# Optimization experiments

Measured on AMD Instinct MI355X. Metric: run time of the kernel, lower is better.

The kernel has to match this reference:

```python
import jax, jax.numpy as jnp
import numpy as np

EPS = 1e-05


def setup_inputs() -> dict:
    key = jax.random.key(0)
    k0, k1, k2, k3, k4 = jax.random.split(key, 5)
    B, N, D = 8, 4096, 1024
    scale = 1.0 / np.sqrt(D)  # roughly xavier scale for D x D
    return {
        "x": jax.random.normal(k0, (B, N, D), dtype=jnp.float32),
        "w_query_real": jax.random.normal(k1, (D, D), dtype=jnp.float32) * scale,
        "w_query_imag": jax.random.normal(k2, (D, D), dtype=jnp.float32) * scale,
        "w_key": jax.random.normal(k3, (D, D), dtype=jnp.float32) * scale,
        "w_value": jax.random.normal(k4, (D, D), dtype=jnp.float32) * scale,
    }


def reference(x, w_query_real, w_query_imag, w_key, w_value):
    # x is real -> x_real = x_imag = x (torch fallback branch)
    q_real = jnp.einsum('bnd,de->bne', x, w_query_real)
    q_imag = jnp.einsum('bnd,de->bne', x, w_query_imag)
    query = jax.nn.relu(q_real) * jax.nn.relu(q_imag)  # relu gating; dropout p=0

    key = jnp.einsum('bnd,de->bne', x, w_key)
    value = jnp.einsum('bnd,de->bne', x, w_value)
    # L2 norm over the sequence axis (dim=1), keepdim
    key = key / (jnp.linalg.norm(key, axis=1, keepdims=True) + EPS)
    value = value / (jnp.linalg.norm(value, axis=1, keepdims=True) + EPS)

    kv_attn = jax.nn.relu(jnp.einsum('bnd,bne->bde', key, value))  # [B, D, D]
    return jnp.einsum('bnd,bde->bne', query, kv_attn)
```

## Files before the change

kernel.cpp:

```cpp
#include <hip/hip_runtime.h>
#include <stdint.h>
#include <stddef.h>

#define D_ 1024
#define NSEQ_ 4096
#define BATCH_ 8
#define BN_ (BATCH_ * NSEQ_)

typedef __attribute__((ext_vector_type(8))) short short8;
typedef __attribute__((ext_vector_type(4))) short short4_t;
typedef __attribute__((ext_vector_type(4))) float float4_t;

__device__ __forceinline__ short f2b(float f) {
  union { float f; uint32_t u; } x; x.f = f;
  uint32_t r = x.u + 0x7fffu + ((x.u >> 16) & 1u);
  return (short)(r >> 16);
}
__device__ __forceinline__ float b2f(short s) {
  union { float f; uint32_t u; } x; x.u = ((uint32_t)(uint16_t)s) << 16; return x.f;
}

__device__ __forceinline__ void gll16(const void* g, void* l) {
  auto gp = reinterpret_cast<const uint32_t __attribute__((address_space(1)))*>(
      reinterpret_cast<uintptr_t>(g));
  auto lp = reinterpret_cast<uint32_t __attribute__((address_space(3)))*>(
      reinterpret_cast<uintptr_t>(l));
  __builtin_amdgcn_global_load_lds(gp, lp, 16, 0, 0);
}

#define MFMA16(a, b, c) __builtin_amdgcn_mfma_f32_16x16x32_bf16(a, b, c, 0, 0, 0)

__global__ void convert_x(const float* __restrict__ X, short* __restrict__ Xb) {
  const size_t i = (size_t)blockIdx.x * 256 + threadIdx.x;
  const float4_t* p = (const float4_t*)(X + i * 8);
  float4_t a = p[0], b = p[1];
  short8 o;
  o[0] = f2b(a.x); o[1] = f2b(a.y); o[2] = f2b(a.z); o[3] = f2b(a.w);
  o[4] = f2b(b.x); o[5] = f2b(b.y); o[6] = f2b(b.z); o[7] = f2b(b.w);
  *(short8*)(Xb + i * 8) = o;
}

__global__ void transpose_convert_w(const float* __restrict__ w0, const float* __restrict__ w1,
                                    const float* __restrict__ w2, const float* __restrict__ w3,
                                    short* __restrict__ wT) {
  __shared__ float tile[32][33];
  const int z = blockIdx.z;
  const float* src = (z == 0) ? w0 : (z == 1) ? w1 : (z == 2) ? w2 : w3;
  short* dst = wT + (size_t)z * D_ * D_;
  const int d0 = blockIdx.y * 32, e0 = blockIdx.x * 32;
  const int tx = threadIdx.x, ty = threadIdx.y;
#pragma unroll
  for (int i = 0; i < 4; ++i) {
    int d = ty + i * 8;
    tile[d][tx] = src[(size_t)(d0 + d) * D_ + (e0 + tx)];
  }
  __syncthreads();
#pragma unroll
  for (int i = 0; i < 4; ++i) {
    int e = ty + i * 8;
    dst[(size_t)(e0 + e) * D_ + (d0 + tx)] = f2b(tile[tx][e]);
  }
}

__global__ __launch_bounds__(256, 2) void gemm_x2w(
    const short* __restrict__ Xb,
    const short* __restrict__ W0, const short* __restrict__ W1,
    short* __restrict__ out0, short* __restrict__ out1,
    float* __restrict__ ss0, float* __restrict__ ss1, int mode) {
  __shared__ union {
    struct { short As[128 * 32]; short Bs[2 * 64 * 32]; } s;
    short T[64 * 136];
  } u;

  const int t = threadIdx.x;
  const int w = t >> 6;
  const int lane = t & 63;
  const int l16 = lane & 15;
  const int quad = lane >> 4;
  const int wm = w >> 1, wn = w & 1;
  const int M0 = blockIdx.y * 128;
  const int E0 = blockIdx.x * 64;

  const float4_t fz = {0.f, 0.f, 0.f, 0.f};
  float4_t acc[2][4][2];
#pragma unroll
  for (int a = 0; a < 2; ++a)
#pragma unroll
    for (int i = 0; i < 4; ++i)
#pragma unroll
      for (int j = 0; j < 2; ++j) acc[a][i][j] = fz;

  const int rowq = lane >> 2;
  const int chunk = (lane & 3) * 8;

  for (int k0 = 0; k0 < 1024; k0 += 32) {
#pragma unroll
    for (int r = 0; r < 4; ++r) {
      const int q = w * 4 + r;
      if (q < 8) {
        gll16(Xb + (size_t)(M0 + q * 16 + rowq) * 1024 + (k0 + chunk), &u.s.As[q * 512]);
      } else {
        const int qq = q - 8;
        const int wt = qq >> 2;
        const int row = (qq & 3) * 16 + rowq;
        gll16((wt ? W1 : W0) + (size_t)(E0 + row) * 1024 + (k0 + chunk),
              &u.s.Bs[qq * 512]);
      }
    }
    __syncthreads();
    short8 aF[4], b0F[2], b1F[2];
#pragma unroll
    for (int i = 0; i < 4; ++i)
      aF[i] = *(const short8*)&u.s.As[(wm * 64 + i * 16 + l16) * 32 + quad * 8];
#pragma unroll
    for (int j = 0; j < 2; ++j) {
      b0F[j] = *(const short8*)&u.s.Bs[(wn * 32 + j * 16 + l16) * 32 + quad * 8];
      b1F[j] = *(const short8*)&u.s.Bs[2048 + (wn * 32 + j * 16 + l16) * 32 + quad * 8];
    }
#pragma unroll
    for (int i = 0; i < 4; ++i)
#pragma unroll
      for (int j = 0; j < 2; ++j) {
        acc[0][i][j] = MFMA16(aF[i], b0F[j], acc[0][i][j]);
        acc[1][i][j] = MFMA16(aF[i], b1F[j], acc[1][i][j]);
      }
    __syncthreads();
  }

  if (mode == 0) {
#pragma unroll
    for (int i = 0; i < 4; ++i) {
      const int rowb = M0 + wm * 64 + i * 16 + quad * 4;
#pragma unroll
      for (int j = 0; j < 2; ++j) {
        const int col = E0 + wn * 32 + j * 16 + l16;
#pragma unroll
        for (int rr = 0; rr < 4; ++rr) {
          float v = fmaxf(acc[0][i][j][rr], 0.f) * fmaxf(acc[1][i][j][rr], 0.f);
          out0[(size_t)(rowb + rr) * 1024 + col] = f2b(v);
        }
      }
    }
  } else {
    const int b = M0 >> 12;
    const int n0 = M0 & 4095;
#pragma unroll
    for (int wt = 0; wt < 2; ++wt) {
      short* dst = wt ? out1 : out0;
      float* ss = wt ? ss1 : ss0;
      __syncthreads();
#pragma unroll
      for (int i = 0; i < 4; ++i) {
        const int rowl = wm * 64 + i * 16 + quad * 4;
#pragma unroll
        for (int j = 0; j < 2; ++j) {
          const int coll = wn * 32 + j * 16 + l16;
#pragma unroll
          for (int rr = 0; rr < 4; ++rr)
            u.T[coll * 136 + rowl + rr] = f2b(acc[wt][i][j][rr]);
        }
      }
      __syncthreads();
#pragma unroll
      for (int it = 0; it < 4; ++it) {
        const int e = it * 16 + (t >> 4);
        const int mchunk = (t & 15) * 8;
        short8 vv = *(const short8*)&u.T[e * 136 + mchunk];
        *(short8*)&dst[((size_t)b * 1024 + E0 + e) * 4096 + n0 + mchunk] = vv;
        float s = 0.f;
#pragma unroll
        for (int x2 = 0; x2 < 8; ++x2) { float f = b2f(vv[x2]); s += f * f; }
        s += __shfl_xor(s, 1, 16);
        s += __shfl_xor(s, 2, 16);
        s += __shfl_xor(s, 4, 16);
        s += __shfl_xor(s, 8, 16);
        if ((t & 15) == 0) atomicAdd(&ss[b * 1024 + E0 + e], s);
      }
    }
  }
}

__global__ void finish_norms(const float* __restrict__ ss, float* __restrict__ inv) {
  const int i = blockIdx.x * 256 + threadIdx.x;
  if (i < 2 * BATCH_ * D_) inv[i] = 1.f / (sqrtf(ss[i]) + 1e-5f);
}

__global__ __launch_bounds__(256, 2) void gemm_bt(
    const short* __restrict__ A, const short* __restrict__ Bm,
    size_t sAb, size_t sBb, int K, int mode,
    const float* __restrict__ rsb, const float* __restrict__ csb,
    void* __restrict__ outp) {
  __shared__ short As[128 * 32];
  __shared__ short Bs[128 * 32];
  const int t = threadIdx.x;
  const int w = t >> 6;
  const int lane = t & 63;
  const int l16 = lane & 15;
  const int quad = lane >> 4;
  const int wm = w >> 1, wn = w & 1;
  const int M0 = blockIdx.y * 128, N0 = blockIdx.x * 128, b = blockIdx.z;
  const short* Ab = A + (size_t)b * sAb;
  const short* Bb = Bm + (size_t)b * sBb;

  const float4_t fz = {0.f, 0.f, 0.f, 0.f};
  float4_t acc[4][4];
#pragma unroll
  for (int i = 0; i < 4; ++i)
#pragma unroll
    for (int j = 0; j < 4; ++j) acc[i][j] = fz;

  const int rowq = lane >> 2;
  const int chunk = (lane & 3) * 8;

  for (int k0 = 0; k0 < K; k0 += 32) {
#pragma unroll
    for (int r = 0; r < 4; ++r) {
      const int q = w * 4 + r;
      if (q < 8) {
        const int row = q * 16 + rowq;
        gll16(Ab + (size_t)(M0 + row) * K + (k0 + chunk), &As[q * 512]);
      } else {
        const int row = (q - 8) * 16 + rowq;
        gll16(Bb + (size_t)(N0 + row) * K + (k0 + chunk), &Bs[(q - 8) * 512]);
      }
    }
    __syncthreads();
    short8 aF[4], bF[4];
#pragma unroll
    for (int i = 0; i < 4; ++i)
      aF[i] = *(const short8*)&As[(wm * 64 + i * 16 + l16) * 32 + quad * 8];
#pragma unroll
    for (int j = 0; j < 4; ++j)
      bF[j] = *(const short8*)&Bs[(wn * 64 + j * 16 + l16) * 32 + quad * 8];
#pragma unroll
    for (int i = 0; i < 4; ++i)
#pragma unroll
      for (int j = 0; j < 4; ++j) acc[i][j] = MFMA16(aF[i], bF[j], acc[i][j]);
    __syncthreads();
  }

  if (mode == 0) {
    short* ob = (short*)outp + (size_t)b * D_ * D_;
    const float* rs = rsb + b * D_ + M0;
    const float* cs = csb + b * D_ + N0;
#pragma unroll
    for (int i = 0; i < 4; ++i) {
      const int rl = wm * 64 + i * 16 + quad * 4;
#pragma unroll
      for (int j = 0; j < 4; ++j) {
        const int cl = wn * 64 + j * 16 + l16;
        const float csc = cs[cl];
#pragma unroll
        for (int rr = 0; rr < 4; ++rr) {
          float v = acc[i][j][rr] * rs[rl + rr] * csc;
          v = fmaxf(v, 0.f);
          ob[(size_t)(M0 + rl + rr) * 1024 + (N0 + cl)] = f2b(v);
        }
      }
    }
  } else {
    float* of = (float*)outp + (size_t)b * NSEQ_ * D_;
#pragma unroll
    for (int i = 0; i < 4; ++i) {
      const int rl = wm * 64 + i * 16 + quad * 4;
#pragma unroll
      for (int j = 0; j < 4; ++j) {
        const int cl = wn * 64 + j * 16 + l16;
#pragma unroll
        for (int rr = 0; rr < 4; ++rr)
          of[(size_t)(M0 + rl + rr) * 1024 + (N0 + cl)] = acc[i][j][rr];
      }
    }
  }
}

extern "C" void kernel_launch(void* const* d_in, const int* in_sizes, int n_in,
                              void* d_out, int out_size, void* d_ws, size_t ws_size,
                              hipStream_t stream) {
  const float* x = (const float*)d_in[0];
  const float* wqr = (const float*)d_in[1];
  const float* wqi = (const float*)d_in[2];
  const float* wk = (const float*)d_in[3];
  const float* wv = (const float*)d_in[4];

  short* wT = (short*)d_ws;
  short* qb = wT + (size_t)4 * D_ * D_;
  short* kT = qb + (size_t)BN_ * D_;
  short* vT = kT + (size_t)BATCH_ * D_ * NSEQ_;
  short* kvT = vT + (size_t)BATCH_ * D_ * NSEQ_;
  float* ssk = (float*)(kvT + (size_t)BATCH_ * D_ * D_);
  float* ssv = ssk + BATCH_ * D_;
  float* invk = ssv + BATCH_ * D_;
  float* invv = invk + BATCH_ * D_;

  short* xb = (short*)d_out;

  hipMemsetAsync(ssk, 0, (size_t)2 * BATCH_ * D_ * sizeof(float), stream);

  convert_x<<<dim3(16384), 256, 0, stream>>>(x, xb);

  transpose_convert_w<<<dim3(32, 32, 4), dim3(32, 8), 0, stream>>>(wqr, wqi, wk, wv, wT);

  gemm_x2w<<<dim3(16, 256), 256, 0, stream>>>(
      xb, wT, wT + (size_t)D_ * D_, qb, nullptr, nullptr, nullptr, 0);
  gemm_x2w<<<dim3(16, 256), 256, 0, stream>>>(
      xb, wT + (size_t)2 * D_ * D_, wT + (size_t)3 * D_ * D_, kT, vT, ssk, ssv, 1);

  finish_norms<<<dim3(64), 256, 0, stream>>>(ssk, invk);

  gemm_bt<<<dim3(8, 8, 8), 256, 0, stream>>>(
      vT, kT, (size_t)D_ * NSEQ_, (size_t)D_ * NSEQ_, 4096, 0, invv, invk, (void*)kvT);

  gemm_bt<<<dim3(8, 32, 8), 256, 0, stream>>>(
      qb, kvT, (size_t)NSEQ_ * D_, (size_t)D_ * D_, 1024, 1, nullptr, nullptr, d_out);
}
```

Measured before the change: 804.1 us.

## Fuse the four x·W projection GEMMs into one kernel sharing the X tile

```diff
diff --git a/kernel.cpp b/kernel.cpp
--- a/kernel.cpp
+++ b/kernel.cpp
@@ -62,13 +62,12 @@
   }
 }
 
-__global__ __launch_bounds__(256, 2) void gemm_x2w(
-    const short* __restrict__ Xb,
-    const short* __restrict__ W0, const short* __restrict__ W1,
-    short* __restrict__ out0, short* __restrict__ out1,
-    float* __restrict__ ss0, float* __restrict__ ss1, int mode) {
+__global__ __launch_bounds__(256, 2) void gemm_x4w(
+    const short* __restrict__ Xb, const short* __restrict__ Wall,
+    short* __restrict__ qout, short* __restrict__ kT, short* __restrict__ vT,
+    float* __restrict__ ssk, float* __restrict__ ssv) {
   __shared__ union {
-    struct { short As[128 * 32]; short Bs[2 * 64 * 32]; } s;
+    struct { short As[128 * 32]; short Bs[4 * 64 * 32]; } s;
     short T[64 * 136];
   } u;
 
@@ -82,9 +81,9 @@
   const int E0 = blockIdx.x * 64;
 
   const float4_t fz = {0.f, 0.f, 0.f, 0.f};
-  float4_t acc[2][4][2];
-#pragma unroll
-  for (int a = 0; a < 2; ++a)
+  float4_t acc[4][4][2];
+#pragma unroll
+  for (int a = 0; a < 4; ++a)
 #pragma unroll
     for (int i = 0; i < 4; ++i)
 #pragma unroll
@@ -95,87 +94,84 @@
 
   for (int k0 = 0; k0 < 1024; k0 += 32) {
 #pragma unroll
-    for (int r = 0; r < 4; ++r) {
-      const int q = w * 4 + r;
+    for (int r = 0; r < 6; ++r) {
+      const int q = w * 6 + r;
       if (q < 8) {
         gll16(Xb + (size_t)(M0 + q * 16 + rowq) * 1024 + (k0 + chunk), &u.s.As[q * 512]);
       } else {
         const int qq = q - 8;
-        const int wt = qq >> 2;
-        const int row = (qq & 3) * 16 + rowq;
-        gll16((wt ? W1 : W0) + (size_t)(E0 + row) * 1024 + (k0 + chunk),
+        gll16(Wall + (size_t)(qq >> 2) * D_ * D_ +
+                  (size_t)(E0 + (qq & 3) * 16 + rowq) * 1024 + (k0 + chunk),
               &u.s.Bs[qq * 512]);
       }
     }
     __syncthreads();
-    short8 aF[4], b0F[2], b1F[2];
+    short8 aF[4], bF[4][2];
 #pragma unroll
     for (int i = 0; i < 4; ++i)
       aF[i] = *(const short8*)&u.s.As[(wm * 64 + i * 16 + l16) * 32 + quad * 8];
 #pragma unroll
+    for (int wt = 0; wt < 4; ++wt)
+#pragma unroll
+      for (int j = 0; j < 2; ++j)
+        bF[wt][j] = *(const short8*)&u.s.Bs[wt * 2048 + (wn * 32 + j * 16 + l16) * 32 + quad * 8];
+#pragma unroll
+    for (int i = 0; i < 4; ++i)
+#pragma unroll
+      for (int wt = 0; wt < 4; ++wt)
+#pragma unroll
+        for (int j = 0; j < 2; ++j)
+          acc[wt][i][j] = MFMA16(aF[i], bF[wt][j], acc[wt][i][j]);
+    __syncthreads();
+  }
+
+#pragma unroll
+  for (int i = 0; i < 4; ++i) {
+    const int rowb = M0 + wm * 64 + i * 16 + quad * 4;
+#pragma unroll
     for (int j = 0; j < 2; ++j) {
-      b0F[j] = *(const short8*)&u.s.Bs[(wn * 32 + j * 16 + l16) * 32 + quad * 8];
-      b1F[j] = *(const short8*)&u.s.Bs[2048 + (wn * 32 + j * 16 + l16) * 32 + quad * 8];
-    }
-#pragma unroll
-    for (int i = 0; i < 4; ++i)
+      const int col = E0 + wn * 32 + j * 16 + l16;
+#pragma unroll
+      for (int rr = 0; rr < 4; ++rr) {
+        float v = fmaxf(acc[0][i][j][rr], 0.f) * fmaxf(acc[1][i][j][rr], 0.f);
+        qout[(size_t)(rowb + rr) * 1024 + col] = f2b(v);
+      }
+    }
+  }
+
+  const int b = M0 >> 12;
+  const int n0 = M0 & 4095;
+#pragma unroll
+  for (int wt = 2; wt < 4; ++wt) {
+    short* dst = (wt == 2) ? kT : vT;
+    float* ss = (wt == 2) ? ssk : ssv;
+    if (wt == 3) __syncthreads();
+#pragma unroll
+    for (int i = 0; i < 4; ++i) {
+      const int rowl = wm * 64 + i * 16 + quad * 4;
 #pragma unroll
       for (int j = 0; j < 2; ++j) {
-        acc[0][i][j] = MFMA16(aF[i], b0F[j], acc[0][i][j]);
-        acc[1][i][j] = MFMA16(aF[i], b1F[j], acc[1][i][j]);
-      }
-    __syncthreads();
-  }
-
-  if (mode == 0) {
-#pragma unroll
-    for (int i = 0; i < 4; ++i) {
-      const int rowb = M0 + wm * 64 + i * 16 + quad * 4;
-#pragma unroll
-      for (int j = 0; j < 2; ++j) {
-        const int col = E0 + wn * 32 + j * 16 + l16;
-#pragma unroll
-        for (int rr = 0; rr < 4; ++rr) {
-          float v = fmaxf(acc[0][i][j][rr], 0.f) * fmaxf(acc[1][i][j][rr], 0.f);
-          out0[(size_t)(rowb + rr) * 1024 + col] = f2b(v);
-        }
-      }
-    }
-  } else {
-    const int b = M0 >> 12;
-    const int n0 = M0 & 4095;
-#pragma unroll
-    for (int wt = 0; wt < 2; ++wt) {
-      short* dst = wt ? out1 : out0;
-      float* ss = wt ? ss1 : ss0;
-      __syncthreads();
-#pragma unroll
-      for (int i = 0; i < 4; ++i) {
-        const int rowl = wm * 64 + i * 16 + quad * 4;
-#pragma unroll
-        for (int j = 0; j < 2; ++j) {
-          const int coll = wn * 32 + j * 16 + l16;
-#pragma unroll
-          for (int rr = 0; rr < 4; ++rr)
-            u.T[coll * 136 + rowl + rr] = f2b(acc[wt][i][j][rr]);
-        }
-      }
-      __syncthreads();
-#pragma unroll
-      for (int it = 0; it < 4; ++it) {
-        const int e = it * 16 + (t >> 4);
-        const int mchunk = (t & 15) * 8;
-        short8 vv = *(const short8*)&u.T[e * 136 + mchunk];
-        *(short8*)&dst[((size_t)b * 1024 + E0 + e) * 4096 + n0 + mchunk] = vv;
-        float s = 0.f;
-#pragma unroll
-        for (int x2 = 0; x2 < 8; ++x2) { float f = b2f(vv[x2]); s += f * f; }
-        s += __shfl_xor(s, 1, 16);
-        s += __shfl_xor(s, 2, 16);
-        s += __shfl_xor(s, 4, 16);
-        s += __shfl_xor(s, 8, 16);
-        if ((t & 15) == 0) atomicAdd(&ss[b * 1024 + E0 + e], s);
-      }
+        const int coll = wn * 32 + j * 16 + l16;
+#pragma unroll
+        for (int rr = 0; rr < 4; ++rr)
+          u.T[coll * 136 + rowl + rr] = f2b(acc[wt][i][j][rr]);
+      }
+    }
+    __syncthreads();
+#pragma unroll
+    for (int it = 0; it < 4; ++it) {
+      const int e = it * 16 + (t >> 4);
+      const int mchunk = (t & 15) * 8;
+      short8 vv = *(const short8*)&u.T[e * 136 + mchunk];
+      *(short8*)&dst[((size_t)b * 1024 + E0 + e) * 4096 + n0 + mchunk] = vv;
+      float s = 0.f;
+#pragma unroll
+      for (int x2 = 0; x2 < 8; ++x2) { float f = b2f(vv[x2]); s += f * f; }
+      s += __shfl_xor(s, 1, 16);
+      s += __shfl_xor(s, 2, 16);
+      s += __shfl_xor(s, 4, 16);
+      s += __shfl_xor(s, 8, 16);
+      if ((t & 15) == 0) atomicAdd(&ss[b * 1024 + E0 + e], s);
     }
   }
 }
@@ -301,10 +297,7 @@
 
   transpose_convert_w<<<dim3(32, 32, 4), dim3(32, 8), 0, stream>>>(wqr, wqi, wk, wv, wT);
 
-  gemm_x2w<<<dim3(16, 256), 256, 0, stream>>>(
-      xb, wT, wT + (size_t)D_ * D_, qb, nullptr, nullptr, nullptr, 0);
-  gemm_x2w<<<dim3(16, 256), 256, 0, stream>>>(
-      xb, wT + (size_t)2 * D_ * D_, wT + (size_t)3 * D_ * D_, kT, vT, ssk, ssv, 1);
+  gemm_x4w<<<dim3(16, 256), 256, 0, stream>>>(xb, wT, qb, kT, vT, ssk, ssv);
 
   finish_norms<<<dim3(64), 256, 0, stream>>>(ssk, invk);
 
```

Result: faster. 777.1 us (-3.3%).
